# Optimization experiments

Measured on AMD Instinct MI355X. Metric: run time of the kernel, lower is better.

Reference implementation:

```python
import jax, jax.numpy as jnp
import numpy as np

B, C, H, W = 16, 256, 64, 64
CI = 128  # inter_channels = in_channels // 2
BN_EPS = 1e-5


def _conv1x1(t, w, b):
    # 1x1 conv: t [B,Cin,H,W], w [Cout,Cin], b [Cout]
    return jnp.einsum('bchw,dc->bdhw', t, w) + b[None, :, None, None]


def _maxpool2(t):
    # 2x2 max pool, stride 2: [B,C,H,W] -> [B,C,H/2,W/2]
    b, c, h, w = t.shape
    return t.reshape(b, c, h // 2, 2, w // 2, 2).max(axis=(3, 5))


def setup_inputs() -> dict:
    key = jax.random.key(0)
    ks = jax.random.split(key, 8)
    s = lambda k, shape: (jax.random.normal(k, shape, jnp.float32) * 0.05)
    return {
        'x': jax.random.normal(ks[0], (B, C, H, W), jnp.float32),
        'theta_w': s(ks[1], (CI, C)), 'theta_b': s(ks[2], (CI,)),
        'phi_w': s(ks[3], (CI, C)), 'phi_b': s(ks[4], (CI,)),
        'g_w': s(ks[5], (CI, C)), 'g_b': s(ks[6], (CI,)),
        'W_w': s(ks[7], (C, CI)), 'W_b': jnp.zeros((C,), jnp.float32),
        'bn_gamma': jnp.ones((C,), jnp.float32),
        'bn_beta': jnp.zeros((C,), jnp.float32),
    }


def reference(x, theta_w, theta_b, phi_w, phi_b, g_w, g_b, W_w, W_b, bn_gamma, bn_beta):
    b, c, h, w = x.shape
    ci = theta_w.shape[0]
    # theta (query): [B, N, Ci], N = H*W
    theta_x = _conv1x1(x, theta_w, theta_b).reshape(b, ci, h * w).transpose(0, 2, 1)
    # phi (key), sub-sampled: [B, Ci, M], M = H*W/4
    phi_x = _maxpool2(_conv1x1(x, phi_w, phi_b)).reshape(b, ci, -1)
    # g (value), sub-sampled: [B, M, Ci]
    g_x = _maxpool2(_conv1x1(x, g_w, g_b)).reshape(b, ci, -1).transpose(0, 2, 1)
    # affinity [B, N, M], normalized by number of key positions (f.size(-1))
    f_div_C = jnp.einsum('bnc,bcm->bnm', theta_x, phi_x) / phi_x.shape[-1]
    # weighted aggregation: [B, N, Ci]
    y = jnp.einsum('bnm,bmc->bnc', f_div_C, g_x)
    y = y.transpose(0, 2, 1).reshape(b, ci, h, w)
    # output projection (1x1 conv) + BatchNorm (training-mode batch stats)
    w_y = _conv1x1(y, W_w, W_b)
    mean = w_y.mean(axis=(0, 2, 3), keepdims=True)
    var = w_y.var(axis=(0, 2, 3), keepdims=True)
    w_y = (w_y - mean) * jax.lax.rsqrt(var + BN_EPS)
    w_y = w_y * bn_gamma[None, :, None, None] + bn_beta[None, :, None, None]
    return w_y + x
```

## Files before the change

### kernel.cpp

```cpp
#include <hip/hip_runtime.h>

#define DEVI static __device__ __forceinline__

typedef __attribute__((ext_vector_type(8))) short bf16x8;
typedef __attribute__((ext_vector_type(4))) float f32x4;

DEVI ushort f2bf(float f) {
  union { float f; unsigned u; } v; v.f = f;
  unsigned r = v.u + 0x7fffu + ((v.u >> 16) & 1u);
  return (ushort)(r >> 16);
}
DEVI float bf2f(ushort u) {
  union { unsigned u; float f; } v; v.u = ((unsigned)u) << 16;
  return v.f;
}

#define WS_XT    0ull
#define WS_WCAT  33554432ull
#define WS_PG    (WS_WCAT + 131072ull)
#define WS_RST   (WS_PG + 1048576ull)
#define WS_S     (WS_RST + 2097152ull)
#define WS_WY    (WS_S + 16384ull)
#define WS_SUM   (WS_WY + 33554432ull)
#define WS_PHI   WS_WY
#define WS_G     (WS_WY + 8388608ull)

__global__ __launch_bounds__(256) void kprep(
    const float* __restrict__ x, const float* __restrict__ phw,
    const float* __restrict__ gww, char* __restrict__ ws) {
  __shared__ float tile[64 * 65];
  const int bid = blockIdx.x, t = threadIdx.x;
  if (bid < 4096) {
    const int b = bid >> 8, rem = bid & 255;
    const int c0 = (rem >> 6) * 64, n0 = (rem & 63) * 64;
    const float* xb = x + ((size_t)(b * 256 + c0)) * 4096 + n0;
#pragma unroll
    for (int it = 0; it < 4; ++it) {
      int ch = t + it * 256;
      int cr = ch >> 4, nf = ch & 15;
      float4 v = *(const float4*)(xb + (size_t)cr * 4096 + nf * 4);
      tile[cr * 65 + nf * 4 + 0] = v.x;
      tile[cr * 65 + nf * 4 + 1] = v.y;
      tile[cr * 65 + nf * 4 + 2] = v.z;
      tile[cr * 65 + nf * 4 + 3] = v.w;
    }
    __syncthreads();
    ushort* xT = (ushort*)(ws + WS_XT);
#pragma unroll
    for (int it = 0; it < 2; ++it) {
      int ch = t + it * 256;
      int rn = ch >> 3, jc = ch & 7;
      uint4 pk;
      pk.x = (unsigned)f2bf(tile[(jc * 8 + 0) * 65 + rn]) | ((unsigned)f2bf(tile[(jc * 8 + 1) * 65 + rn]) << 16);
      pk.y = (unsigned)f2bf(tile[(jc * 8 + 2) * 65 + rn]) | ((unsigned)f2bf(tile[(jc * 8 + 3) * 65 + rn]) << 16);
      pk.z = (unsigned)f2bf(tile[(jc * 8 + 4) * 65 + rn]) | ((unsigned)f2bf(tile[(jc * 8 + 5) * 65 + rn]) << 16);
      pk.w = (unsigned)f2bf(tile[(jc * 8 + 6) * 65 + rn]) | ((unsigned)f2bf(tile[(jc * 8 + 7) * 65 + rn]) << 16);
      *(uint4*)(xT + ((size_t)(b * 4096 + n0 + rn)) * 256 + c0 + jc * 8) = pk;
    }
  } else if (bid == 4096) {
    ushort* Wcat = (ushort*)(ws + WS_WCAT);
    for (int idx = t; idx < 65536; idx += 256) {
      int ci = idx >> 8, c = idx & 255;
      float v = (ci < 128) ? phw[ci * 256 + c] : gww[(ci - 128) * 256 + c];
      Wcat[idx] = f2bf(v);
    }
  } else {
    float4 z = {0.f, 0.f, 0.f, 0.f};
    float4* st = (float4*)(ws + WS_SUM);
    if (t < 128) st[t] = z;
  }
}

__global__ __launch_bounds__(256) void kconvpg(
    const float* __restrict__ phib, const float* __restrict__ gb,
    char* __restrict__ ws) {
  __shared__ __align__(16) char lds[49152];
  const int t = threadIdx.x;
  const int b = blockIdx.y, nb = blockIdx.x;
  const int n0 = nb * 128;
  const int lane = t & 63, wave = t >> 6;
  const int lr = lane & 15, lq = lane >> 4;
  const ushort* xT = (const ushort*)(ws + WS_XT) + ((size_t)(b * 4096 + n0)) * 256;
  const ushort* Wc = (const ushort*)(ws + WS_WCAT);

  f32x4 acc[8][4];
#pragma unroll
  for (int i = 0; i < 8; ++i)
#pragma unroll
    for (int j = 0; j < 4; ++j) acc[i][j] = (f32x4){0.f, 0.f, 0.f, 0.f};

  int4 ra[4], rb[8];
#pragma unroll
  for (int it = 0; it < 4; ++it) {
    int ch = t + it * 256, r = ch >> 3, jc = ch & 7;
    ra[it] = *(const int4*)(xT + (size_t)r * 256 + jc * 8);
  }
#pragma unroll
  for (int it = 0; it < 8; ++it) {
    int ch = t + it * 256, r = ch >> 3, jc = ch & 7;
    rb[it] = *(const int4*)(Wc + r * 256 + jc * 8);
  }
  const int swz = (lr & 7) << 4;

  for (int ks = 0; ks < 4; ++ks) {
#pragma unroll
    for (int it = 0; it < 4; ++it) {
      int ch = t + it * 256, r = ch >> 3, jc = ch & 7;
      *(int4*)(lds + r * 128 + ((jc * 16) ^ ((r & 7) << 4))) = ra[it];
    }
#pragma unroll
    for (int it = 0; it < 8; ++it) {
      int ch = t + it * 256, r = ch >> 3, jc = ch & 7;
      *(int4*)(lds + 16384 + r * 128 + ((jc * 16) ^ ((r & 7) << 4))) = rb[it];
    }
    __syncthreads();
    if (ks < 3) {
#pragma unroll
      for (int it = 0; it < 4; ++it) {
        int ch = t + it * 256, r = ch >> 3, jc = ch & 7;
        ra[it] = *(const int4*)(xT + (size_t)r * 256 + (ks + 1) * 64 + jc * 8);
      }
#pragma unroll
      for (int it = 0; it < 8; ++it) {
        int ch = t + it * 256, r = ch >> 3, jc = ch & 7;
        rb[it] = *(const int4*)(Wc + r * 256 + (ks + 1) * 64 + jc * 8);
      }
    }
#pragma unroll
    for (int k2 = 0; k2 < 2; ++k2) {
      const int kb = k2 * 64 + lq * 16;
      bf16x8 bfr[4];
#pragma unroll
      for (int j = 0; j < 4; ++j) {
        int bc = wave * 64 + j * 16 + lr;
        bfr[j] = *(const bf16x8*)(lds + 16384 + bc * 128 + (kb ^ swz));
      }
#pragma unroll
      for (int i = 0; i < 8; ++i) {
        int arw = i * 16 + lr;
        bf16x8 af = *(const bf16x8*)(lds + arw * 128 + (kb ^ swz));
#pragma unroll
        for (int j = 0; j < 4; ++j)
          acc[i][j] = __builtin_amdgcn_mfma_f32_16x16x32_bf16(af, bfr[j], acc[i][j], 0, 0, 0);
      }
    }
    __syncthreads();
  }
#pragma unroll
  for (int j = 0; j < 4; ++j) {
    int cir = wave * 64 + j * 16 + lr;
    float bias;
    float* dst;
    if (cir < 128) {
      bias = phib[cir];
      dst = (float*)(ws + WS_PHI) + ((size_t)(b * 128 + cir)) * 1024;
    } else {
      bias = gb[cir - 128];
      dst = (float*)(ws + WS_G) + ((size_t)(b * 128 + cir - 128)) * 1024;
    }
    dst += nb * 32;
#pragma unroll
    for (int i = 0; i < 4; ++i) {
      f32x4 lo = acc[i][j], hi = acc[i + 4][j];
      float2 m;
      m.x = fmaxf(fmaxf(lo[0], lo[1]), fmaxf(hi[0], hi[1])) + bias;
      m.y = fmaxf(fmaxf(lo[2], lo[3]), fmaxf(hi[2], hi[3])) + bias;
      *(float2*)(dst + i * 8 + lq * 2) = m;
    }
  }
}

__global__ __launch_bounds__(256) void kpg32(char* __restrict__ ws) {
  __shared__ float lphi[32 * 65];
  __shared__ float lgd[32 * 65];
  const int t = threadIdx.x, b = blockIdx.y;
  const int cib = blockIdx.x >> 2, cjb = blockIdx.x & 3;
  const int ci_l = t >> 5, cj_l = t & 31;
  const float* phi = (const float*)(ws + WS_PHI) + ((size_t)(b * 128 + cib * 32)) * 1024;
  const float* gg = (const float*)(ws + WS_G) + ((size_t)(b * 128 + cjb * 32)) * 1024;
  float acc[4] = {0.f, 0.f, 0.f, 0.f};
  for (int kc = 0; kc < 16; ++kc) {
#pragma unroll
    for (int it = 0; it < 8; ++it) {
      int fi = t + it * 256;
      int r = fi >> 6, c = fi & 63;
      lphi[r * 65 + c] = phi[(size_t)r * 1024 + kc * 64 + c];
      lgd[r * 65 + c] = gg[(size_t)r * 1024 + kc * 64 + c];
    }
    __syncthreads();
#pragma unroll 8
    for (int k = 0; k < 64; ++k) {
      float gv = lgd[cj_l * 65 + k];
#pragma unroll
      for (int p = 0; p < 4; ++p)
        acc[p] += lphi[(ci_l * 4 + p) * 65 + k] * gv;
    }
    __syncthreads();
  }
  float* PG = (float*)(ws + WS_PG) + (size_t)b * 16384;
#pragma unroll
  for (int p = 0; p < 4; ++p)
    PG[(cib * 32 + ci_l * 4 + p) * 128 + cjb * 32 + cj_l] = acc[p];
}

__global__ __launch_bounds__(256) void kmid(
    const float* __restrict__ thw, const float* __restrict__ thb,
    const float* __restrict__ wbias, const float* __restrict__ www,
    char* __restrict__ ws) {
  __shared__ __align__(16) char smid[49920];
  float* PGc = (float*)smid;
  float* Wws = (float*)(smid + 16896);
  float* Qts = (float*)(smid + 33408);
  float* thws = (float*)smid;
  const int t = threadIdx.x, b = blockIdx.y, cblk = blockIdx.x;
  const int c_l = t >> 3, q = t & 7;
  const float* PGg = (const float*)(ws + WS_PG) + (size_t)b * 16384;

#pragma unroll
  for (int it = 0; it < 16; ++it) {
    int fi = t + it * 256;
    int r = fi >> 7, j = fi & 127;
    Wws[r * 129 + j] = www[(cblk * 32 + r) * 128 + j];
  }
  float qacc[16];
#pragma unroll
  for (int i = 0; i < 16; ++i) qacc[i] = 0.f;

  for (int jc = 0; jc < 4; ++jc) {
#pragma unroll
    for (int it = 0; it < 16; ++it) {
      int fi = t + it * 256;
      int i = fi >> 5, jl = fi & 31;
      PGc[i * 33 + jl] = PGg[i * 128 + jc * 32 + jl];
    }
    __syncthreads();
#pragma unroll
    for (int iq = 0; iq < 16; ++iq) {
      int i = iq * 8 + q;
      float a = 0.f;
#pragma unroll 8
      for (int jl = 0; jl < 32; ++jl)
        a += Wws[c_l * 129 + jc * 32 + jl] * PGc[i * 33 + jl];
      qacc[iq] += a;
    }
    __syncthreads();
  }
  const float inv = 1.0f / 1024.0f;
#pragma unroll
  for (int iq = 0; iq < 16; ++iq) Qts[c_l * 129 + iq * 8 + q] = qacc[iq] * inv;
  __syncthreads();
  if (t < 32) {
    float sv = wbias[cblk * 32 + t];
    for (int i = 0; i < 128; ++i) sv += thb[i] * Qts[t * 129 + i];
    ((float*)(ws + WS_S))[b * 256 + cblk * 32 + t] = sv;
  }
  ushort* Rstb = (ushort*)(ws + WS_RST) + (size_t)b * 65536;
  for (int cpc = 0; cpc < 4; ++cpc) {
#pragma unroll
    for (int it = 0; it < 32; ++it) {
      int fi = t + it * 256;
      int i = fi >> 6, cp = fi & 63;
      thws[i * 65 + cp] = thw[i * 256 + cpc * 64 + cp];
    }
    __syncthreads();
#pragma unroll
    for (int k = 0; k < 8; ++k) {
      int cpl = q * 8 + k;
      float a = 0.f;
#pragma unroll 8
      for (int i = 0; i < 128; ++i)
        a += Qts[c_l * 129 + i] * thws[i * 65 + cpl];
      Rstb[(cblk * 32 + c_l) * 256 + cpc * 64 + cpl] = f2bf(a);
    }
    __syncthreads();
  }
}

__global__ __launch_bounds__(256) void kwy(char* __restrict__ ws) {
  __shared__ __align__(16) char lds[49152];
  const int t = threadIdx.x;
  const int b = blockIdx.y, nb = blockIdx.x;
  const int n0 = nb * 128;
  const int lane = t & 63, wave = t >> 6;
  const int lr = lane & 15, lq = lane >> 4;
  const ushort* xT = (const ushort*)(ws + WS_XT) + ((size_t)(b * 4096 + n0)) * 256;
  const ushort* Rst = (const ushort*)(ws + WS_RST) + (size_t)b * 65536;
  const float* sarr = (const float*)(ws + WS_S) + b * 256;
  float sreg[4];
#pragma unroll
  for (int j = 0; j < 4; ++j) sreg[j] = sarr[wave * 64 + j * 16 + lr];

  f32x4 acc[8][4];
#pragma unroll
  for (int i = 0; i < 8; ++i)
#pragma unroll
    for (int j = 0; j < 4; ++j) acc[i][j] = (f32x4){0.f, 0.f, 0.f, 0.f};

  int4 ra[4], rb[8];
#pragma unroll
  for (int it = 0; it < 4; ++it) {
    int ch = t + it * 256, r = ch >> 3, jc = ch & 7;
    ra[it] = *(const int4*)(xT + (size_t)r * 256 + jc * 8);
  }
#pragma unroll
  for (int it = 0; it < 8; ++it) {
    int ch = t + it * 256, r = ch >> 3, jc = ch & 7;
    rb[it] = *(const int4*)(Rst + r * 256 + jc * 8);
  }
  const int swz = (lr & 7) << 4;

  for (int ks = 0; ks < 4; ++ks) {
#pragma unroll
    for (int it = 0; it < 4; ++it) {
      int ch = t + it * 256, r = ch >> 3, jc = ch & 7;
      *(int4*)(lds + r * 128 + ((jc * 16) ^ ((r & 7) << 4))) = ra[it];
    }
#pragma unroll
    for (int it = 0; it < 8; ++it) {
      int ch = t + it * 256, r = ch >> 3, jc = ch & 7;
      *(int4*)(lds + 16384 + r * 128 + ((jc * 16) ^ ((r & 7) << 4))) = rb[it];
    }
    __syncthreads();
    if (ks < 3) {
#pragma unroll
      for (int it = 0; it < 4; ++it) {
        int ch = t + it * 256, r = ch >> 3, jc = ch & 7;
        ra[it] = *(const int4*)(xT + (size_t)r * 256 + (ks + 1) * 64 + jc * 8);
      }
#pragma unroll
      for (int it = 0; it < 8; ++it) {
        int ch = t + it * 256, r = ch >> 3, jc = ch & 7;
        rb[it] = *(const int4*)(Rst + r * 256 + (ks + 1) * 64 + jc * 8);
      }
    }
#pragma unroll
    for (int k2 = 0; k2 < 2; ++k2) {
      const int kb = k2 * 64 + lq * 16;
      bf16x8 bfr[4];
#pragma unroll
      for (int j = 0; j < 4; ++j) {
        int bc = wave * 64 + j * 16 + lr;
        bfr[j] = *(const bf16x8*)(lds + 16384 + bc * 128 + (kb ^ swz));
      }
#pragma unroll
      for (int i = 0; i < 8; ++i) {
        int arw = i * 16 + lr;
        bf16x8 af = *(const bf16x8*)(lds + arw * 128 + (kb ^ swz));
#pragma unroll
        for (int j = 0; j < 4; ++j)
          acc[i][j] = __builtin_amdgcn_mfma_f32_16x16x32_bf16(af, bfr[j], acc[i][j], 0, 0, 0);
      }
    }
    __syncthreads();
  }
  ushort* wyp = (ushort*)(ws + WS_WY) + ((size_t)(b * 4096 + n0)) * 256;
  float s1[4] = {0.f, 0.f, 0.f, 0.f}, s2[4] = {0.f, 0.f, 0.f, 0.f};
#pragma unroll
  for (int j = 0; j < 4; ++j) {
#pragma unroll
    for (int i = 0; i < 8; ++i) {
#pragma unroll
      for (int rr = 0; rr < 4; ++rr) {
        int ln = i * 16 + lq * 4 + rr;
        float v = acc[i][j][rr] + sreg[j];
        s1[j] += v;
        s2[j] += v * v;
        wyp[(size_t)ln * 256 + wave * 64 + j * 16 + lr] = f2bf(v);
      }
    }
  }
  float* gsum = (float*)(ws + WS_SUM);
  float* gsq = gsum + 256;
#pragma unroll
  for (int j = 0; j < 4; ++j) {
    float a = s1[j], qv = s2[j];
    a += __shfl_xor(a, 16);
    a += __shfl_xor(a, 32);
    qv += __shfl_xor(qv, 16);
    qv += __shfl_xor(qv, 32);
    if (lq == 0) {
      int c = wave * 64 + j * 16 + lr;
      atomicAdd(&gsum[c], a);
      atomicAdd(&gsq[c], qv);
    }
  }
}

__global__ __launch_bounds__(256) void kout(
    const float* __restrict__ x, const float* __restrict__ gamma,
    const float* __restrict__ beta, const char* __restrict__ ws,
    float* __restrict__ out) {
  __shared__ float tile[256 * 35];
  __shared__ float scaleL[256], shiftL[256];
  const int t = threadIdx.x;
  const int b = blockIdx.y, n0 = blockIdx.x * 32;
  const ushort* wy = (const ushort*)(ws + WS_WY) + ((size_t)(b * 4096 + n0)) * 256;
#pragma unroll
  for (int it = 0; it < 4; ++it) {
    int ch = t + it * 256;
    int r = ch >> 5, j = ch & 31;
    bf16x8 v = *(const bf16x8*)(wy + (size_t)r * 256 + j * 8);
#pragma unroll
    for (int e = 0; e < 8; ++e) tile[(j * 8 + e) * 35 + r] = bf2f((ushort)v[e]);
  }
  {
    const float* gsum = (const float*)(ws + WS_SUM);
    float sm = gsum[t], sq = gsum[256 + t];
    float mean = sm * (1.0f / 65536.0f);
    float var = sq * (1.0f / 65536.0f) - mean * mean;
    float rs = rsqrtf(var + 1e-5f);
    float sc = gamma[t] * rs;
    scaleL[t] = sc;
    shiftL[t] = beta[t] - mean * sc;
  }
  __syncthreads();
  const float* xb = x + (size_t)b * 1048576 + n0;
  float* ob = out + (size_t)b * 1048576 + n0;
#pragma unroll
  for (int it = 0; it < 8; ++it) {
    int ch = t + it * 256;
    int c = ch >> 3, nj = ch & 7;
    float4 xv = *(const float4*)(xb + (size_t)c * 4096 + nj * 4);
    float sc = scaleL[c], sh = shiftL[c];
    float4 ov;
    ov.x = tile[c * 35 + nj * 4 + 0] * sc + sh + xv.x;
    ov.y = tile[c * 35 + nj * 4 + 1] * sc + sh + xv.y;
    ov.z = tile[c * 35 + nj * 4 + 2] * sc + sh + xv.z;
    ov.w = tile[c * 35 + nj * 4 + 3] * sc + sh + xv.w;
    *(float4*)(ob + (size_t)c * 4096 + nj * 4) = ov;
  }
}

extern "C" void kernel_launch(void* const* d_in, const int* in_sizes, int n_in,
                              void* d_out, int out_size, void* d_ws, size_t ws_size,
                              hipStream_t stream) {
  const float* x = (const float*)d_in[0];
  const float* thw = (const float*)d_in[1];
  const float* thb = (const float*)d_in[2];
  const float* phw = (const float*)d_in[3];
  const float* phb = (const float*)d_in[4];
  const float* gw = (const float*)d_in[5];
  const float* gb = (const float*)d_in[6];
  const float* www = (const float*)d_in[7];
  const float* wwb = (const float*)d_in[8];
  const float* gamma = (const float*)d_in[9];
  const float* beta = (const float*)d_in[10];
  char* ws = (char*)d_ws;
  float* out = (float*)d_out;

  kprep<<<dim3(4098), dim3(256), 0, stream>>>(x, phw, gw, ws);
  kconvpg<<<dim3(32, 16), dim3(256), 0, stream>>>(phb, gb, ws);
  kpg32<<<dim3(16, 16), dim3(256), 0, stream>>>(ws);
  kmid<<<dim3(8, 16), dim3(256), 0, stream>>>(thw, thb, wwb, www, ws);
  kwy<<<dim3(32, 16), dim3(256), 0, stream>>>(ws);
  kout<<<dim3(128, 16), dim3(256), 0, stream>>>(x, gamma, beta, ws, out);
}
```

Before: 416.2 us.

## Store wy channel-major, split-K pg32 with atomics, coalesce pooled phi/g stores

The projection kernel is transposed so each block covers 64 positions by 256 channels and writes wy in channel-major layout. Stores are staged through LDS and written coalesced, and per-channel BN sums are computed there. The output kernel then does a plain streaming elementwise pass with no LDS transpose. The phi·g reduction kernel is split along K into four slices that accumulate with atomics into a buffer zeroed in the prep kernel, which adds parallelism. Pooled phi/g outputs are also staged through LDS for float4 coalesced writes. The cost is extra atomics, more blocks, and nondeterministic float summation order.

```diff
diff --git a/kernel.cpp b/kernel.cpp
--- a/kernel.cpp
+++ b/kernel.cpp
@@ -64,10 +64,15 @@
       float v = (ci < 128) ? phw[ci * 256 + c] : gww[(ci - 128) * 256 + c];
       Wcat[idx] = f2bf(v);
     }
-  } else {
+  } else if (bid == 4097) {
     float4 z = {0.f, 0.f, 0.f, 0.f};
     float4* st = (float4*)(ws + WS_SUM);
     if (t < 128) st[t] = z;
+  } else {
+    const int b = bid - 4098;
+    float4 z = {0.f, 0.f, 0.f, 0.f};
+    float4* pg = (float4*)(ws + WS_PG + (size_t)b * 65536);
+    for (int i = t; i < 4096; i += 256) pg[i] = z;
   }
 }
 
@@ -146,40 +151,43 @@
     }
     __syncthreads();
   }
+  float* pool = (float*)lds;
 #pragma unroll
   for (int j = 0; j < 4; ++j) {
     int cir = wave * 64 + j * 16 + lr;
-    float bias;
-    float* dst;
-    if (cir < 128) {
-      bias = phib[cir];
-      dst = (float*)(ws + WS_PHI) + ((size_t)(b * 128 + cir)) * 1024;
-    } else {
-      bias = gb[cir - 128];
-      dst = (float*)(ws + WS_G) + ((size_t)(b * 128 + cir - 128)) * 1024;
-    }
-    dst += nb * 32;
+    float bias = (cir < 128) ? phib[cir] : gb[cir - 128];
 #pragma unroll
     for (int i = 0; i < 4; ++i) {
       f32x4 lo = acc[i][j], hi = acc[i + 4][j];
-      float2 m;
-      m.x = fmaxf(fmaxf(lo[0], lo[1]), fmaxf(hi[0], hi[1])) + bias;
-      m.y = fmaxf(fmaxf(lo[2], lo[3]), fmaxf(hi[2], hi[3])) + bias;
-      *(float2*)(dst + i * 8 + lq * 2) = m;
-    }
+      float m0 = fmaxf(fmaxf(lo[0], lo[1]), fmaxf(hi[0], hi[1])) + bias;
+      float m1 = fmaxf(fmaxf(lo[2], lo[3]), fmaxf(hi[2], hi[3])) + bias;
+      pool[cir * 36 + i * 8 + lq * 2] = m0;
+      pool[cir * 36 + i * 8 + lq * 2 + 1] = m1;
+    }
+  }
+  __syncthreads();
+  const int rr_ = t >> 3, chk = t & 7;
+#pragma unroll
+  for (int pass = 0; pass < 8; ++pass) {
+    int ci = pass * 32 + rr_;
+    float4 v = *(const float4*)(pool + ci * 36 + chk * 4);
+    float* dst = (ci < 128)
+        ? ((float*)(ws + WS_PHI) + ((size_t)(b * 128 + ci)) * 1024)
+        : ((float*)(ws + WS_G) + ((size_t)(b * 128 + ci - 128)) * 1024);
+    *(float4*)(dst + nb * 32 + chk * 4) = v;
   }
 }
 
 __global__ __launch_bounds__(256) void kpg32(char* __restrict__ ws) {
   __shared__ float lphi[32 * 65];
   __shared__ float lgd[32 * 65];
-  const int t = threadIdx.x, b = blockIdx.y;
+  const int t = threadIdx.x, b = blockIdx.y, kz = blockIdx.z;
   const int cib = blockIdx.x >> 2, cjb = blockIdx.x & 3;
   const int ci_l = t >> 5, cj_l = t & 31;
   const float* phi = (const float*)(ws + WS_PHI) + ((size_t)(b * 128 + cib * 32)) * 1024;
   const float* gg = (const float*)(ws + WS_G) + ((size_t)(b * 128 + cjb * 32)) * 1024;
   float acc[4] = {0.f, 0.f, 0.f, 0.f};
-  for (int kc = 0; kc < 16; ++kc) {
+  for (int kc = kz * 4; kc < kz * 4 + 4; ++kc) {
 #pragma unroll
     for (int it = 0; it < 8; ++it) {
       int fi = t + it * 256;
@@ -200,7 +208,7 @@
   float* PG = (float*)(ws + WS_PG) + (size_t)b * 16384;
 #pragma unroll
   for (int p = 0; p < 4; ++p)
-    PG[(cib * 32 + ci_l * 4 + p) * 128 + cjb * 32 + cj_l] = acc[p];
+    atomicAdd(&PG[(cib * 32 + ci_l * 4 + p) * 128 + cjb * 32 + cj_l], acc[p]);
 }
 
 __global__ __launch_bounds__(256) void kmid(
@@ -276,61 +284,56 @@
   }
 }
 
-__global__ __launch_bounds__(256) void kwy(char* __restrict__ ws) {
-  __shared__ __align__(16) char lds[49152];
+__global__ __launch_bounds__(256) void kwyT(char* __restrict__ ws) {
+  __shared__ __align__(16) char lds[40960];
   const int t = threadIdx.x;
   const int b = blockIdx.y, nb = blockIdx.x;
-  const int n0 = nb * 128;
+  const int n0 = nb * 64;
   const int lane = t & 63, wave = t >> 6;
   const int lr = lane & 15, lq = lane >> 4;
   const ushort* xT = (const ushort*)(ws + WS_XT) + ((size_t)(b * 4096 + n0)) * 256;
   const ushort* Rst = (const ushort*)(ws + WS_RST) + (size_t)b * 65536;
-  const float* sarr = (const float*)(ws + WS_S) + b * 256;
-  float sreg[4];
-#pragma unroll
-  for (int j = 0; j < 4; ++j) sreg[j] = sarr[wave * 64 + j * 16 + lr];
-
-  f32x4 acc[8][4];
-#pragma unroll
-  for (int i = 0; i < 8; ++i)
+
+  f32x4 acc[4][4];
+#pragma unroll
+  for (int i = 0; i < 4; ++i)
 #pragma unroll
     for (int j = 0; j < 4; ++j) acc[i][j] = (f32x4){0.f, 0.f, 0.f, 0.f};
 
-  int4 ra[4], rb[8];
-#pragma unroll
-  for (int it = 0; it < 4; ++it) {
-    int ch = t + it * 256, r = ch >> 3, jc = ch & 7;
-    ra[it] = *(const int4*)(xT + (size_t)r * 256 + jc * 8);
-  }
+  int4 ra[8], rb[2];
 #pragma unroll
   for (int it = 0; it < 8; ++it) {
     int ch = t + it * 256, r = ch >> 3, jc = ch & 7;
-    rb[it] = *(const int4*)(Rst + r * 256 + jc * 8);
-  }
-  const int swz = (lr & 7) << 4;
+    ra[it] = *(const int4*)(Rst + r * 256 + jc * 8);
+  }
+#pragma unroll
+  for (int it = 0; it < 2; ++it) {
+    int ch = t + it * 256, r = ch >> 3, jc = ch & 7;
+    rb[it] = *(const int4*)(xT + (size_t)r * 256 + jc * 8);
+  }
 
   for (int ks = 0; ks < 4; ++ks) {
 #pragma unroll
-    for (int it = 0; it < 4; ++it) {
+    for (int it = 0; it < 8; ++it) {
       int ch = t + it * 256, r = ch >> 3, jc = ch & 7;
       *(int4*)(lds + r * 128 + ((jc * 16) ^ ((r & 7) << 4))) = ra[it];
     }
 #pragma unroll
-    for (int it = 0; it < 8; ++it) {
+    for (int it = 0; it < 2; ++it) {
       int ch = t + it * 256, r = ch >> 3, jc = ch & 7;
-      *(int4*)(lds + 16384 + r * 128 + ((jc * 16) ^ ((r & 7) << 4))) = rb[it];
+      *(int4*)(lds + 32768 + r * 128 + ((jc * 16) ^ ((r & 7) << 4))) = rb[it];
     }
     __syncthreads();
     if (ks < 3) {
-#pragma unroll
-      for (int it = 0; it < 4; ++it) {
-        int ch = t + it * 256, r = ch >> 3, jc = ch & 7;
-        ra[it] = *(const int4*)(xT + (size_t)r * 256 + (ks + 1) * 64 + jc * 8);
-      }
 #pragma unroll
       for (int it = 0; it < 8; ++it) {
         int ch = t + it * 256, r = ch >> 3, jc = ch & 7;
-        rb[it] = *(const int4*)(Rst + r * 256 + (ks + 1) * 64 + jc * 8);
+        ra[it] = *(const int4*)(Rst + r * 256 + (ks + 1) * 64 + jc * 8);
+      }
+#pragma unroll
+      for (int it = 0; it < 2; ++it) {
+        int ch = t + it * 256, r = ch >> 3, jc = ch & 7;
+        rb[it] = *(const int4*)(xT + (size_t)r * 256 + (ks + 1) * 64 + jc * 8);
       }
     }
 #pragma unroll
@@ -339,13 +342,13 @@
       bf16x8 bfr[4];
 #pragma unroll
       for (int j = 0; j < 4; ++j) {
-        int bc = wave * 64 + j * 16 + lr;
-        bfr[j] = *(const bf16x8*)(lds + 16384 + bc * 128 + (kb ^ swz));
-      }
-#pragma unroll
-      for (int i = 0; i < 8; ++i) {
-        int arw = i * 16 + lr;
-        bf16x8 af = *(const bf16x8*)(lds + arw * 128 + (kb ^ swz));
+        int rn = j * 16 + lr;
+        bfr[j] = *(const bf16x8*)(lds + 32768 + rn * 128 + (kb ^ ((rn & 7) << 4)));
+      }
+#pragma unroll
+      for (int i = 0; i < 4; ++i) {
+        int rc = wave * 64 + i * 16 + lr;
+        bf16x8 af = *(const bf16x8*)(lds + rc * 128 + (kb ^ ((rc & 7) << 4)));
 #pragma unroll
         for (int j = 0; j < 4; ++j)
           acc[i][j] = __builtin_amdgcn_mfma_f32_16x16x32_bf16(af, bfr[j], acc[i][j], 0, 0, 0);
@@ -353,35 +356,46 @@
     }
     __syncthreads();
   }
-  ushort* wyp = (ushort*)(ws + WS_WY) + ((size_t)(b * 4096 + n0)) * 256;
-  float s1[4] = {0.f, 0.f, 0.f, 0.f}, s2[4] = {0.f, 0.f, 0.f, 0.f};
-#pragma unroll
-  for (int j = 0; j < 4; ++j) {
-#pragma unroll
-    for (int i = 0; i < 8; ++i) {
+  ushort* po = (ushort*)lds;
+#pragma unroll
+  for (int i = 0; i < 4; ++i)
+#pragma unroll
+    for (int j = 0; j < 4; ++j)
 #pragma unroll
       for (int rr = 0; rr < 4; ++rr) {
-        int ln = i * 16 + lq * 4 + rr;
-        float v = acc[i][j][rr] + sreg[j];
-        s1[j] += v;
-        s2[j] += v * v;
-        wyp[(size_t)ln * 256 + wave * 64 + j * 16 + lr] = f2bf(v);
-      }
-    }
-  }
+        int c_ = wave * 64 + i * 16 + lq * 4 + rr;
+        po[c_ * 72 + j * 16 + lr] = f2bf(acc[i][j][rr]);
+      }
+  __syncthreads();
+  const float* sarr = (const float*)(ws + WS_S) + b * 256;
+  ushort* wyb = (ushort*)(ws + WS_WY) + (size_t)b * 1048576;
   float* gsum = (float*)(ws + WS_SUM);
   float* gsq = gsum + 256;
-#pragma unroll
-  for (int j = 0; j < 4; ++j) {
-    float a = s1[j], qv = s2[j];
-    a += __shfl_xor(a, 16);
-    a += __shfl_xor(a, 32);
-    qv += __shfl_xor(qv, 16);
-    qv += __shfl_xor(qv, 32);
-    if (lq == 0) {
-      int c = wave * 64 + j * 16 + lr;
-      atomicAdd(&gsum[c], a);
-      atomicAdd(&gsq[c], qv);
+  const int rr_ = t >> 3, chk = t & 7;
+#pragma unroll
+  for (int pass = 0; pass < 8; ++pass) {
+    int c = pass * 32 + rr_;
+    int4 v = *(const int4*)(po + c * 72 + chk * 8);
+    float sv = sarr[c];
+    unsigned w[4] = {(unsigned)v.x, (unsigned)v.y, (unsigned)v.z, (unsigned)v.w};
+    float s1 = 0.f, s2 = 0.f;
+    unsigned o[4];
+#pragma unroll
+    for (int q = 0; q < 4; ++q) {
+      float f0 = bf2f((ushort)(w[q] & 0xffffu)) + sv;
+      float f1 = bf2f((ushort)(w[q] >> 16)) + sv;
+      s1 += f0 + f1;
+      s2 += f0 * f0 + f1 * f1;
+      o[q] = (unsigned)f2bf(f0) | ((unsigned)f2bf(f1) << 16);
+    }
+    int4 ov;
+    ov.x = (int)o[0]; ov.y = (int)o[1]; ov.z = (int)o[2]; ov.w = (int)o[3];
+    *(int4*)(wyb + (size_t)c * 4096 + n0 + chk * 8) = ov;
+    s1 += __shfl_xor(s1, 1); s1 += __shfl_xor(s1, 2); s1 += __shfl_xor(s1, 4);
+    s2 += __shfl_xor(s2, 1); s2 += __shfl_xor(s2, 2); s2 += __shfl_xor(s2, 4);
+    if (chk == 0) {
+      atomicAdd(&gsum[c], s1);
+      atomicAdd(&gsq[c], s2);
     }
   }
 }
@@ -390,19 +404,9 @@
     const float* __restrict__ x, const float* __restrict__ gamma,
     const float* __restrict__ beta, const char* __restrict__ ws,
     float* __restrict__ out) {
-  __shared__ float tile[256 * 35];
   __shared__ float scaleL[256], shiftL[256];
   const int t = threadIdx.x;
-  const int b = blockIdx.y, n0 = blockIdx.x * 32;
-  const ushort* wy = (const ushort*)(ws + WS_WY) + ((size_t)(b * 4096 + n0)) * 256;
-#pragma unroll
-  for (int it = 0; it < 4; ++it) {
-    int ch = t + it * 256;
-    int r = ch >> 5, j = ch & 31;
-    bf16x8 v = *(const bf16x8*)(wy + (size_t)r * 256 + j * 8);
-#pragma unroll
-    for (int e = 0; e < 8; ++e) tile[(j * 8 + e) * 35 + r] = bf2f((ushort)v[e]);
-  }
+  const int b = blockIdx.y, blk = blockIdx.x;
   {
     const float* gsum = (const float*)(ws + WS_SUM);
     float sm = gsum[t], sq = gsum[256 + t];
@@ -414,20 +418,22 @@
     shiftL[t] = beta[t] - mean * sc;
   }
   __syncthreads();
-  const float* xb = x + (size_t)b * 1048576 + n0;
-  float* ob = out + (size_t)b * 1048576 + n0;
+  const ushort* wyb = (const ushort*)(ws + WS_WY) + (size_t)b * 1048576;
+  const float* xb = x + (size_t)b * 1048576;
+  float* ob = out + (size_t)b * 1048576;
 #pragma unroll
   for (int it = 0; it < 8; ++it) {
-    int ch = t + it * 256;
-    int c = ch >> 3, nj = ch & 7;
-    float4 xv = *(const float4*)(xb + (size_t)c * 4096 + nj * 4);
+    int idx = blk * 8192 + it * 1024 + t * 4;
+    int c = idx >> 12;
+    uint2 wv = *(const uint2*)(wyb + idx);
+    float4 xv = *(const float4*)(xb + idx);
     float sc = scaleL[c], sh = shiftL[c];
     float4 ov;
-    ov.x = tile[c * 35 + nj * 4 + 0] * sc + sh + xv.x;
-    ov.y = tile[c * 35 + nj * 4 + 1] * sc + sh + xv.y;
-    ov.z = tile[c * 35 + nj * 4 + 2] * sc + sh + xv.z;
-    ov.w = tile[c * 35 + nj * 4 + 3] * sc + sh + xv.w;
-    *(float4*)(ob + (size_t)c * 4096 + nj * 4) = ov;
+    ov.x = bf2f((ushort)(wv.x & 0xffffu)) * sc + sh + xv.x;
+    ov.y = bf2f((ushort)(wv.x >> 16)) * sc + sh + xv.y;
+    ov.z = bf2f((ushort)(wv.y & 0xffffu)) * sc + sh + xv.z;
+    ov.w = bf2f((ushort)(wv.y >> 16)) * sc + sh + xv.w;
+    *(float4*)(ob + idx) = ov;
   }
 }
 
@@ -448,10 +454,10 @@
   char* ws = (char*)d_ws;
   float* out = (float*)d_out;
 
-  kprep<<<dim3(4098), dim3(256), 0, stream>>>(x, phw, gw, ws);
+  kprep<<<dim3(4114), dim3(256), 0, stream>>>(x, phw, gw, ws);
   kconvpg<<<dim3(32, 16), dim3(256), 0, stream>>>(phb, gb, ws);
-  kpg32<<<dim3(16, 16), dim3(256), 0, stream>>>(ws);
+  kpg32<<<dim3(16, 16, 4), dim3(256), 0, stream>>>(ws);
   kmid<<<dim3(8, 16), dim3(256), 0, stream>>>(thw, thb, wwb, www, ws);
-  kwy<<<dim3(32, 16), dim3(256), 0, stream>>>(ws);
+  kwyT<<<dim3(64, 16), dim3(256), 0, stream>>>(ws);
   kout<<<dim3(128, 16), dim3(256), 0, stream>>>(x, gamma, beta, ws, out);
 }
```

Measured after the change: 478.5 us. 15.0% more time.
